# Optimization experiments

Hardware: AMD Instinct MI355X
Metric: run time of the kernel (lower is better)

## Reference

```python
import jax, jax.numpy as jnp
import numpy as np

B, C_IN, C_OUT, L = 16, 512, 512, 2048
HEADS, K, U, KS, PAD = 4, 16, 1, 3, 1
VV = C_OUT // HEADS  # 128
EPS = 1e-5


def _conv1d(x, w, pad):
    # x: [B, Cin, L], w: [Cout, Cin, KS] -> [B, Cout, L]
    return jax.lax.conv_general_dilated(
        x, w, window_strides=(1,), padding=[(pad, pad)],
        dimension_numbers=('NCH', 'OIH', 'NCH'))


def _bn_eval(y, gamma, beta, mean, var):
    # inference-mode BatchNorm1d over channel axis
    scale = gamma * jax.lax.rsqrt(var + EPS)
    shift = beta - mean * scale
    return y * scale[None, :, None] + shift[None, :, None]


def setup_inputs() -> dict:
    key = jax.random.key(0)
    ks = jax.random.split(key, 8)
    std_q = 1.0 / np.sqrt(C_IN * KS)
    x = jax.random.normal(ks[0], (B, C_IN, L), dtype=jnp.float32)
    Wq = jax.random.normal(ks[1], (K * HEADS, C_IN, KS), dtype=jnp.float32) * std_q
    Wk = jax.random.normal(ks[2], (K * U, C_IN, KS), dtype=jnp.float32) * std_q
    Wv = jax.random.normal(ks[3], (VV * U, C_IN, KS), dtype=jnp.float32) * std_q
    embedding = jax.random.normal(ks[4], (K, U), dtype=jnp.float32)
    return {
        'x': x, 'Wq': Wq,
        'q_gamma': jnp.ones((K * HEADS,), jnp.float32),
        'q_beta': jnp.zeros((K * HEADS,), jnp.float32),
        'q_mean': jnp.zeros((K * HEADS,), jnp.float32),
        'q_var': jnp.ones((K * HEADS,), jnp.float32),
        'Wk': Wk, 'Wv': Wv,
        'v_gamma': jnp.ones((VV * U,), jnp.float32),
        'v_beta': jnp.zeros((VV * U,), jnp.float32),
        'v_mean': jnp.zeros((VV * U,), jnp.float32),
        'v_var': jnp.ones((VV * U,), jnp.float32),
        'embedding': embedding,
    }


def reference(x, Wq, q_gamma, q_beta, q_mean, q_var, Wk, Wv,
              v_gamma, v_beta, v_mean, v_var, embedding):
    batch, _, n = x.shape
    # projections
    q = _bn_eval(_conv1d(x, Wq, PAD), q_gamma, q_beta, q_mean, q_var)
    q = q.reshape(batch, HEADS, K, n)                      # bhkn
    keys = _conv1d(x, Wk, PAD).reshape(batch, K, U, n)     # bkun
    sm = jax.nn.softmax(keys, axis=-1)                     # softmax over positions
    v = _bn_eval(_conv1d(x, Wv, PAD), v_gamma, v_beta, v_mean, v_var)
    v = v.reshape(batch, VV, U, n)                         # bvun
    # content lambda
    lambda_c = jnp.einsum('bkun,bvun->bkv', sm, v)
    y_c = jnp.einsum('bhkn,bkv->bhvn', q, lambda_c)
    # position lambda
    lambda_p = jnp.einsum('ku,bvun->bkvn', embedding, v)
    y_p = jnp.einsum('bhkn,bkvn->bhvn', q, lambda_p)
    out = y_c + y_p
    return out.reshape(batch, HEADS * VV, n)
```

## Files before the change

### kernel.cpp

```cpp
#include <hip/hip_runtime.h>
#include <hip/hip_bf16.h>

#define BB 16
#define CIN 512
#define LLN 2048
#define EPSV 1e-5f
#define WIMG_U16 6144

typedef __attribute__((ext_vector_type(8))) short bf16x8s;
typedef __attribute__((ext_vector_type(4))) float f32x4;

__device__ __forceinline__ unsigned short f2bf(float f) {
    union { float f; unsigned int i; } c; c.f = f;
    unsigned int x = c.i;
    unsigned int lsb = (x >> 16) & 1;
    x += 0x7fff + lsb;
    return (unsigned short)(x >> 16);
}
__device__ __forceinline__ float bf2f(unsigned short u) {
    union { unsigned int i; float f; } c; c.i = ((unsigned int)u) << 16; return c.f;
}
__device__ __forceinline__ float bflo(unsigned int w) {
    union { unsigned int i; float f; } c; c.i = w << 16; return c.f;
}
__device__ __forceinline__ float bfhi(unsigned int w) {
    union { unsigned int i; float f; } c; c.i = w & 0xffff0000u; return c.f;
}
__device__ __forceinline__ unsigned int cvtpk2(float a, float b) {
    union { __hip_bfloat162 h; unsigned int u; } c;
    c.h = __float22bfloat162_rn(float2{a, b});
    return c.u;
}

__device__ __forceinline__ void g2l16(const void* g, void* l) {
    typedef const __attribute__((address_space(1))) unsigned int GU;
    typedef __attribute__((address_space(3))) unsigned int LU;
    __builtin_amdgcn_global_load_lds((GU*)g, (LU*)l, 16, 0, 0);
}

__global__ __launch_bounds__(256) void prep_w(
    const float* __restrict__ Wq, const float* __restrict__ Wk,
    const float* __restrict__ Wv, unsigned short* __restrict__ Wpk)
{
    const int tid = threadIdx.x;
    const int wblk = blockIdx.y * 8 + blockIdx.x;
    const int img = wblk >> 1, half = wblk & 1;
    const int cot = img >> 4, chunk = img & 15;
    const int ci0 = chunk * 32;
    for (int i = half * 3072 + tid; i < half * 3072 + 3072; i += 256) {
        int t = i >> 11, r = i & 2047;
        int cf = r >> 9, lane = (r >> 3) & 63, e = i & 7;
        int lm = lane & 15, kq = lane >> 4;
        int cop = cot * 64 + cf * 16 + lm;
        int cig = ci0 + kq * 8 + e;
        float val = 0.f;
        if (cop < 64)        val = Wq[((size_t)cop * 512 + cig) * 3 + t];
        else if (cop < 80)   val = Wk[((size_t)(cop - 64) * 512 + cig) * 3 + t];
        else if (cop < 208)  val = Wv[((size_t)(cop - 80) * 512 + cig) * 3 + t];
        Wpk[(size_t)img * WIMG_U16 + i] = f2bf(val);
    }
}

__global__ __launch_bounds__(512, 4) void conv_mfma(
    const float* __restrict__ x, const unsigned short* __restrict__ Wpk,
    const float* __restrict__ qg, const float* __restrict__ qb,
    const float* __restrict__ qm, const float* __restrict__ qv,
    const float* __restrict__ vg, const float* __restrict__ vb,
    const float* __restrict__ vm, const float* __restrict__ vvar,
    unsigned short* __restrict__ qb16, float* __restrict__ kbuf,
    unsigned short* __restrict__ vb16)
{
    __shared__ __align__(16) unsigned short xT[258 * 32];
    __shared__ __align__(16) unsigned short wA[2][WIMG_U16];
    __shared__ __align__(16) float xs32[32 * 256];
    __shared__ float sscale[64], sshift[64];

    const int tid = threadIdx.x;
    const int wave = tid >> 6, lane = tid & 63;
    const int kq = lane >> 4, lm = lane & 15;
    const int n0 = blockIdx.x * 256;
    const int cot = blockIdx.y;
    const int b = blockIdx.z;

    const float* xb = x + (size_t)b * CIN * LLN;
    const unsigned short* wbase = Wpk + (size_t)cot * 16 * WIMG_U16;

    float hl0 = 0.f, hl1 = 0.f;

#define STAGE_X32(chunk)                                                        \
    {                                                                           \
        const float* src = xb + (size_t)(chunk) * 32 * LLN + n0;                \
        _Pragma("unroll")                                                       \
        for (int j = 0; j < 4; j++) {                                           \
            int i = tid + j * 512;                                              \
            g2l16(src + (size_t)(i >> 6) * LLN + (i & 63) * 4,                  \
                  (char*)xs32 + (size_t)i * 16);                                \
        }                                                                       \
    }
#define STAGE_W(buf, chunk)                                                     \
    {                                                                           \
        const unsigned short* wsrc = wbase + (size_t)(chunk) * WIMG_U16;        \
        for (int i = tid; i < 768; i += 512)                                    \
            g2l16(wsrc + (size_t)i * 8, &wA[buf][i * 8]);                       \
    }
#define HALO_ISSUE(chunk)                                                       \
    if (tid < 32) {                                                             \
        int side = tid & 1, p = tid >> 1;                                       \
        int nh = side ? (n0 + 256) : (n0 - 1);                                  \
        hl0 = 0.f; hl1 = 0.f;                                                   \
        if (nh >= 0 && nh < LLN) {                                              \
            hl0 = xb[((size_t)(chunk) * 32 + 2 * p) * LLN + nh];                \
            hl1 = xb[((size_t)(chunk) * 32 + 2 * p + 1) * LLN + nh];            \
        }                                                                       \
    }
#define TRANSPOSE()                                                             \
    {                                                                           \
        int nl = tid >> 1, h = tid & 1, rp = nl + 1;                            \
        int sig = (rp >> 1) & 3;                                                \
        unsigned short* row = &xT[rp * 32];                                     \
        _Pragma("unroll")                                                       \
        for (int g2 = 0; g2 < 2; g2++) {                                        \
            int gg = h * 2 + g2;                                                \
            float f0 = xs32[(gg * 8 + 0) * 256 + nl];                           \
            float f1 = xs32[(gg * 8 + 1) * 256 + nl];                           \
            float f2 = xs32[(gg * 8 + 2) * 256 + nl];                           \
            float f3 = xs32[(gg * 8 + 3) * 256 + nl];                           \
            float f4 = xs32[(gg * 8 + 4) * 256 + nl];                           \
            float f5 = xs32[(gg * 8 + 5) * 256 + nl];                           \
            float f6 = xs32[(gg * 8 + 6) * 256 + nl];                           \
            float f7 = xs32[(gg * 8 + 7) * 256 + nl];                           \
            uint4 w = make_uint4(cvtpk2(f0, f1), cvtpk2(f2, f3),                \
                                 cvtpk2(f4, f5), cvtpk2(f6, f7));               \
            *(uint4*)&row[(gg ^ sig) * 8] = w;                                  \
        }                                                                       \
        if (tid < 32) {                                                         \
            int side = tid & 1, p = tid >> 1;                                   \
            int hr = side ? 257 : 0;             \
            *(unsigned int*)&xT[hr * 32 + p * 2] = cvtpk2(hl0, hl1);            \
        }                                                                       \
    }

    STAGE_X32(0) STAGE_W(0, 0) HALO_ISSUE(0)

    if (tid < 64) {
        int cop = cot * 64 + tid;
        float sc = 1.f, sh = 0.f;
        if (cop < 64) {
            float g = qg[cop], be = qb[cop], m = qm[cop], va = qv[cop];
            sc = g * rsqrtf(va + EPSV); sh = be - m * sc;
        } else if (cop >= 80 && cop < 208) {
            int cc = cop - 80;
            float g = vg[cc], be = vb[cc], m = vm[cc], va = vvar[cc];
            sc = g * rsqrtf(va + EPSV); sh = be - m * sc;
        }
        sscale[tid] = sc; sshift[tid] = sh;
    }

    f32x4 acc[4][2];
#pragma unroll
    for (int i = 0; i < 4; i++)
#pragma unroll
        for (int j = 0; j < 2; j++) acc[i][j] = (f32x4){0.f, 0.f, 0.f, 0.f};

    asm volatile("s_waitcnt vmcnt(0)" ::: "memory");
    __syncthreads();
    TRANSPOSE()
    __syncthreads();

    for (int chunk = 0; chunk < 16; chunk++) {
        const int cur = chunk & 1;
        if (chunk < 15) { STAGE_X32(chunk + 1) STAGE_W(cur ^ 1, chunk + 1) HALO_ISSUE(chunk + 1) }

#pragma unroll
        for (int t = 0; t < 3; t++) {
            bf16x8s aF[4];
#pragma unroll
            for (int cf = 0; cf < 4; cf++)
                aF[cf] = *(const bf16x8s*)&wA[cur][((t * 4 + cf) * 64 + lane) * 8];
#pragma unroll
            for (int fn = 0; fn < 2; fn++) {
                int lr = wave * 32 + fn * 16 + lm + t;
                int grp = kq ^ ((lr >> 1) & 3);
                bf16x8s bF = *(const bf16x8s*)&xT[lr * 32 + grp * 8];
#pragma unroll
                for (int cf = 0; cf < 4; cf++)
                    acc[cf][fn] = __builtin_amdgcn_mfma_f32_16x16x32_bf16(
                        aF[cf], bF, acc[cf][fn], 0, 0, 0);
            }
        }
        asm volatile("s_waitcnt vmcnt(0)" ::: "memory");
        __syncthreads();
        if (chunk < 15) { TRANSPOSE() __syncthreads(); }
    }
#undef STAGE_X32
#undef STAGE_W
#undef HALO_ISSUE
#undef TRANSPOSE

#pragma unroll
    for (int cf = 0; cf < 4; cf++) {
#pragma unroll
        for (int fn = 0; fn < 2; fn++) {
#pragma unroll
            for (int r = 0; r < 4; r++) {
                int col = cf * 16 + kq * 4 + r;
                int cop = cot * 64 + col;
                if (cop >= 208) continue;
                float val = acc[cf][fn][r] * sscale[col] + sshift[col];
                int nout = n0 + wave * 32 + fn * 16 + lm;
                if (cop < 64)
                    qb16[((size_t)b * 64 + cop) * LLN + nout] = f2bf(val);
                else if (cop < 80)
                    kbuf[((size_t)b * 16 + (cop - 64)) * LLN + nout] = __expf(val - 16.f);
                else
                    vb16[((size_t)b * 128 + (cop - 80)) * LLN + nout] = f2bf(val);
            }
        }
    }
}

__global__ __launch_bounds__(256) void lambdac_kernel(
    const float* __restrict__ kexp, const unsigned short* __restrict__ vb16,
    float* __restrict__ lc2, float* __restrict__ s2)
{
    const int wave = threadIdx.x >> 6;
    const int lane = threadIdx.x & 63;
    const int idx = blockIdx.x;
    const int half = idx & 1;
    const int vgp = (idx >> 1) & 31;
    const int b = idx >> 6;
    const float* ps = kexp + ((size_t)b * 16 + wave * 4) * LLN + half * 1024;
    const unsigned short* pv = vb16 + ((size_t)b * 128 + vgp * 4) * LLN + half * 1024;

    float sum[4] = {0.f, 0.f, 0.f, 0.f};
    float acc[4][4];
#pragma unroll
    for (int k = 0; k < 4; k++)
#pragma unroll
        for (int v = 0; v < 4; v++) acc[k][v] = 0.f;
#pragma unroll
    for (int j = 0; j < 2; j++) {
        int n = (j * 64 + lane) * 8;
        float e[4][8];
#pragma unroll
        for (int k = 0; k < 4; k++) {
            float4 a = *(const float4*)&ps[(size_t)k * LLN + n];
            float4 c = *(const float4*)&ps[(size_t)k * LLN + n + 4];
            e[k][0] = a.x; e[k][1] = a.y; e[k][2] = a.z; e[k][3] = a.w;
            e[k][4] = c.x; e[k][5] = c.y; e[k][6] = c.z; e[k][7] = c.w;
            sum[k] += a.x + a.y + a.z + a.w + c.x + c.y + c.z + c.w;
        }
#pragma unroll
        for (int v = 0; v < 4; v++) {
            uint4 w = *(const uint4*)&pv[(size_t)v * LLN + n];
            float vv[8] = {bflo(w.x), bfhi(w.x), bflo(w.y), bfhi(w.y),
                           bflo(w.z), bfhi(w.z), bflo(w.w), bfhi(w.w)};
#pragma unroll
            for (int k = 0; k < 4; k++) {
                float t = 0.f;
#pragma unroll
                for (int q = 0; q < 8; q++) t += e[k][q] * vv[q];
                acc[k][v] += t;
            }
        }
    }
#pragma unroll
    for (int k = 0; k < 4; k++) {
#pragma unroll
        for (int off = 32; off > 0; off >>= 1)
            sum[k] += __shfl_xor(sum[k], off, 64);
#pragma unroll
        for (int v = 0; v < 4; v++)
#pragma unroll
            for (int off = 32; off > 0; off >>= 1)
                acc[k][v] += __shfl_xor(acc[k][v], off, 64);
    }
    if (lane == 0) {
#pragma unroll
        for (int k = 0; k < 4; k++) {
#pragma unroll
            for (int v = 0; v < 4; v++)
                lc2[(((size_t)half * 16 + b) * 16 + wave * 4 + k) * 128 + vgp * 4 + v]
                    = acc[k][v];
            if (vgp == 0)
                s2[((size_t)half * 16 + b) * 16 + wave * 4 + k] = sum[k];
        }
    }
}

__global__ __launch_bounds__(256) void final_kernel(
    const unsigned short* __restrict__ qb16, const unsigned short* __restrict__ vb16,
    const float* __restrict__ lc2, const float* __restrict__ s2,
    const float* __restrict__ emb, float* __restrict__ out)
{
    __shared__ float lcsT[64][16];
    __shared__ float es[16], invd[16];
    const int tid = threadIdx.x;
    const int h = tid >> 6, nl = tid & 63;
    const int n0 = blockIdx.x * 64;
    const int vh = blockIdx.y * 64;
    const int b = blockIdx.z;

    if (tid < 16) {
        es[tid] = emb[tid];
        invd[tid] = 1.f / (s2[(size_t)b * 16 + tid] + s2[256 + (size_t)b * 16 + tid]);
    }
    __syncthreads();
    for (int i = tid; i < 1024; i += 256) {
        int k = i & 15, vl = i >> 4;
        float l0 = lc2[((size_t)b * 16 + k) * 128 + vh + vl];
        float l1 = lc2[(size_t)32768 + ((size_t)b * 16 + k) * 128 + vh + vl];
        lcsT[vl][k] = (l0 + l1) * invd[k];
    }
    __syncthreads();

    const int n = n0 + nl;
    const unsigned short* pq = qb16 + ((size_t)b * 64 + h * 16) * LLN + n;
    float4 q4[4];
#pragma unroll
    for (int kk = 0; kk < 4; kk++) {
        q4[kk].x = bf2f(pq[(size_t)(kk * 4 + 0) * LLN]);
        q4[kk].y = bf2f(pq[(size_t)(kk * 4 + 1) * LLN]);
        q4[kk].z = bf2f(pq[(size_t)(kk * 4 + 2) * LLN]);
        q4[kk].w = bf2f(pq[(size_t)(kk * 4 + 3) * LLN]);
    }
    float s = 0.f;
#pragma unroll
    for (int kk = 0; kk < 4; kk++)
        s += q4[kk].x * es[kk * 4] + q4[kk].y * es[kk * 4 + 1]
           + q4[kk].z * es[kk * 4 + 2] + q4[kk].w * es[kk * 4 + 3];

    const unsigned short* pv = vb16 + ((size_t)b * 128 + vh) * LLN + n;
    float* po = out + ((size_t)b * 512 + h * 128 + vh) * LLN + n;
#pragma unroll 4
    for (int v = 0; v < 64; v++) {
        const float* lrow = &lcsT[v][0];
        float4 c0 = *(const float4*)&lrow[0];
        float4 c1 = *(const float4*)&lrow[4];
        float4 c2 = *(const float4*)&lrow[8];
        float4 c3 = *(const float4*)&lrow[12];
        float lam = q4[0].x * c0.x + q4[0].y * c0.y + q4[0].z * c0.z + q4[0].w * c0.w
                  + q4[1].x * c1.x + q4[1].y * c1.y + q4[1].z * c1.z + q4[1].w * c1.w
                  + q4[2].x * c2.x + q4[2].y * c2.y + q4[2].z * c2.z + q4[2].w * c2.w
                  + q4[3].x * c3.x + q4[3].y * c3.y + q4[3].z * c3.z + q4[3].w * c3.w;
        float vvv = bf2f(pv[(size_t)v * LLN]);
        po[(size_t)v * LLN] = lam + s * vvv;
    }
}

extern "C" void kernel_launch(void* const* d_in, const int* in_sizes, int n_in,
                              void* d_out, int out_size, void* d_ws, size_t ws_size,
                              hipStream_t stream)
{
    const float* x   = (const float*)d_in[0];
    const float* Wq  = (const float*)d_in[1];
    const float* qg  = (const float*)d_in[2];
    const float* qb  = (const float*)d_in[3];
    const float* qm  = (const float*)d_in[4];
    const float* qv  = (const float*)d_in[5];
    const float* Wk  = (const float*)d_in[6];
    const float* Wv  = (const float*)d_in[7];
    const float* vg  = (const float*)d_in[8];
    const float* vb  = (const float*)d_in[9];
    const float* vm  = (const float*)d_in[10];
    const float* vva = (const float*)d_in[11];
    const float* emb = (const float*)d_in[12];
    float* out = (float*)d_out;

    float* kbuf = (float*)d_ws;
    float* lc2  = kbuf + (size_t)BB * 16 * LLN;
    float* s2   = lc2 + (size_t)2 * BB * 16 * 128;
    unsigned short* qb16 = (unsigned short*)(s2 + 512);
    unsigned short* vb16 = qb16 + (size_t)BB * 64 * LLN;
    unsigned short* Wpk  = vb16 + (size_t)BB * 128 * LLN;

    hipLaunchKernelGGL(prep_w, dim3(8, 16), dim3(256), 0, stream, Wq, Wk, Wv, Wpk);

    hipLaunchKernelGGL(conv_mfma, dim3(8, 4, 16), dim3(512), 0, stream,
                       x, Wpk, qg, qb, qm, qv, vg, vb, vm, vva,
                       qb16, kbuf, vb16);

    hipLaunchKernelGGL(lambdac_kernel, dim3(1024), dim3(256), 0, stream,
                       kbuf, vb16, lc2, s2);

    hipLaunchKernelGGL(final_kernel, dim3(32, 2, BB), dim3(256), 0, stream,
                       qb16, vb16, lc2, s2, emb, out);
}
```

Baseline: 190.2 us.

## Merge lambda-content and final kernels via grid-wide atomic barrier

Fuses the lambda_c reduction kernel and the output kernel into one persistent launch of 1024 blocks. A global atomic counter, reset by the conv kernel, serves as a grid barrier between the two phases. This removes one kernel launch and the gap between launches. In exchange it relies on all 1024 blocks being co-resident, and it uses a bounded spin guard that could let a block proceed before every block has arrived, giving wrong results.

```diff
diff --git a/kernel.cpp b/kernel.cpp
--- a/kernel.cpp
+++ b/kernel.cpp
@@ -68,7 +68,7 @@
     const float* __restrict__ vg, const float* __restrict__ vb,
     const float* __restrict__ vm, const float* __restrict__ vvar,
     unsigned short* __restrict__ qb16, float* __restrict__ kbuf,
-    unsigned short* __restrict__ vb16)
+    unsigned short* __restrict__ vb16, unsigned int* __restrict__ sync_ctr)
 {
     __shared__ __align__(16) unsigned short xT[258 * 32];
     __shared__ __align__(16) unsigned short wA[2][WIMG_U16];
@@ -81,6 +81,9 @@
     const int n0 = blockIdx.x * 256;
     const int cot = blockIdx.y;
     const int b = blockIdx.z;
+
+    if (blockIdx.x == 0 && blockIdx.y == 0 && blockIdx.z == 0 && tid == 0)
+        *sync_ctr = 0;
 
     const float* xb = x + (size_t)b * CIN * LLN;
     const unsigned short* wbase = Wpk + (size_t)cot * 16 * WIMG_U16;
@@ -219,132 +222,146 @@
     }
 }
 
-__global__ __launch_bounds__(256) void lambdac_kernel(
+__global__ __launch_bounds__(256, 4) void lc_final(
     const float* __restrict__ kexp, const unsigned short* __restrict__ vb16,
-    float* __restrict__ lc2, float* __restrict__ s2)
-{
-    const int wave = threadIdx.x >> 6;
-    const int lane = threadIdx.x & 63;
-    const int idx = blockIdx.x;
-    const int half = idx & 1;
-    const int vgp = (idx >> 1) & 31;
-    const int b = idx >> 6;
-    const float* ps = kexp + ((size_t)b * 16 + wave * 4) * LLN + half * 1024;
-    const unsigned short* pv = vb16 + ((size_t)b * 128 + vgp * 4) * LLN + half * 1024;
-
-    float sum[4] = {0.f, 0.f, 0.f, 0.f};
-    float acc[4][4];
-#pragma unroll
-    for (int k = 0; k < 4; k++)
-#pragma unroll
-        for (int v = 0; v < 4; v++) acc[k][v] = 0.f;
-#pragma unroll
-    for (int j = 0; j < 2; j++) {
-        int n = (j * 64 + lane) * 8;
-        float e[4][8];
-#pragma unroll
-        for (int k = 0; k < 4; k++) {
-            float4 a = *(const float4*)&ps[(size_t)k * LLN + n];
-            float4 c = *(const float4*)&ps[(size_t)k * LLN + n + 4];
-            e[k][0] = a.x; e[k][1] = a.y; e[k][2] = a.z; e[k][3] = a.w;
-            e[k][4] = c.x; e[k][5] = c.y; e[k][6] = c.z; e[k][7] = c.w;
-            sum[k] += a.x + a.y + a.z + a.w + c.x + c.y + c.z + c.w;
-        }
-#pragma unroll
-        for (int v = 0; v < 4; v++) {
-            uint4 w = *(const uint4*)&pv[(size_t)v * LLN + n];
-            float vv[8] = {bflo(w.x), bfhi(w.x), bflo(w.y), bfhi(w.y),
-                           bflo(w.z), bfhi(w.z), bflo(w.w), bfhi(w.w)};
-#pragma unroll
-            for (int k = 0; k < 4; k++) {
-                float t = 0.f;
-#pragma unroll
-                for (int q = 0; q < 8; q++) t += e[k][q] * vv[q];
-                acc[k][v] += t;
-            }
-        }
-    }
-#pragma unroll
-    for (int k = 0; k < 4; k++) {
-#pragma unroll
-        for (int off = 32; off > 0; off >>= 1)
-            sum[k] += __shfl_xor(sum[k], off, 64);
-#pragma unroll
-        for (int v = 0; v < 4; v++)
-#pragma unroll
-            for (int off = 32; off > 0; off >>= 1)
-                acc[k][v] += __shfl_xor(acc[k][v], off, 64);
-    }
-    if (lane == 0) {
-#pragma unroll
-        for (int k = 0; k < 4; k++) {
-#pragma unroll
-            for (int v = 0; v < 4; v++)
-                lc2[(((size_t)half * 16 + b) * 16 + wave * 4 + k) * 128 + vgp * 4 + v]
-                    = acc[k][v];
-            if (vgp == 0)
-                s2[((size_t)half * 16 + b) * 16 + wave * 4 + k] = sum[k];
-        }
-    }
-}
-
-__global__ __launch_bounds__(256) void final_kernel(
-    const unsigned short* __restrict__ qb16, const unsigned short* __restrict__ vb16,
-    const float* __restrict__ lc2, const float* __restrict__ s2,
-    const float* __restrict__ emb, float* __restrict__ out)
+    const unsigned short* __restrict__ qb16, const float* __restrict__ emb,
+    float* __restrict__ lc2, float* __restrict__ s2,
+    unsigned int* __restrict__ sync_ctr, float* __restrict__ out)
 {
     __shared__ float lcsT[64][16];
     __shared__ float es[16], invd[16];
     const int tid = threadIdx.x;
-    const int h = tid >> 6, nl = tid & 63;
-    const int n0 = blockIdx.x * 64;
-    const int vh = blockIdx.y * 64;
-    const int b = blockIdx.z;
-
-    if (tid < 16) {
-        es[tid] = emb[tid];
-        invd[tid] = 1.f / (s2[(size_t)b * 16 + tid] + s2[256 + (size_t)b * 16 + tid]);
-    }
+    const int idx = blockIdx.x;
+
+    {
+        const int wave = tid >> 6;
+        const int lane = tid & 63;
+        const int half = idx & 1;
+        const int vgp = (idx >> 1) & 31;
+        const int b = idx >> 6;
+        const float* ps = kexp + ((size_t)b * 16 + wave * 4) * LLN + half * 1024;
+        const unsigned short* pv = vb16 + ((size_t)b * 128 + vgp * 4) * LLN + half * 1024;
+
+        float sum[4] = {0.f, 0.f, 0.f, 0.f};
+        float acc[4][4];
+#pragma unroll
+        for (int k = 0; k < 4; k++)
+#pragma unroll
+            for (int v = 0; v < 4; v++) acc[k][v] = 0.f;
+#pragma unroll
+        for (int j = 0; j < 2; j++) {
+            int n = (j * 64 + lane) * 8;
+            float e[4][8];
+#pragma unroll
+            for (int k = 0; k < 4; k++) {
+                float4 a = *(const float4*)&ps[(size_t)k * LLN + n];
+                float4 c = *(const float4*)&ps[(size_t)k * LLN + n + 4];
+                e[k][0] = a.x; e[k][1] = a.y; e[k][2] = a.z; e[k][3] = a.w;
+                e[k][4] = c.x; e[k][5] = c.y; e[k][6] = c.z; e[k][7] = c.w;
+                sum[k] += a.x + a.y + a.z + a.w + c.x + c.y + c.z + c.w;
+            }
+#pragma unroll
+            for (int v = 0; v < 4; v++) {
+                uint4 w = *(const uint4*)&pv[(size_t)v * LLN + n];
+                float vv[8] = {bflo(w.x), bfhi(w.x), bflo(w.y), bfhi(w.y),
+                               bflo(w.z), bfhi(w.z), bflo(w.w), bfhi(w.w)};
+#pragma unroll
+                for (int k = 0; k < 4; k++) {
+                    float t = 0.f;
+#pragma unroll
+                    for (int q = 0; q < 8; q++) t += e[k][q] * vv[q];
+                    acc[k][v] += t;
+                }
+            }
+        }
+#pragma unroll
+        for (int k = 0; k < 4; k++) {
+#pragma unroll
+            for (int off = 32; off > 0; off >>= 1)
+                sum[k] += __shfl_xor(sum[k], off, 64);
+#pragma unroll
+            for (int v = 0; v < 4; v++)
+#pragma unroll
+                for (int off = 32; off > 0; off >>= 1)
+                    acc[k][v] += __shfl_xor(acc[k][v], off, 64);
+        }
+        if (lane == 0) {
+#pragma unroll
+            for (int k = 0; k < 4; k++) {
+#pragma unroll
+                for (int v = 0; v < 4; v++)
+                    lc2[(((size_t)half * 16 + b) * 16 + wave * 4 + k) * 128 + vgp * 4 + v]
+                        = acc[k][v];
+                if (vgp == 0)
+                    s2[((size_t)half * 16 + b) * 16 + wave * 4 + k] = sum[k];
+            }
+        }
+    }
+
     __syncthreads();
-    for (int i = tid; i < 1024; i += 256) {
-        int k = i & 15, vl = i >> 4;
-        float l0 = lc2[((size_t)b * 16 + k) * 128 + vh + vl];
-        float l1 = lc2[(size_t)32768 + ((size_t)b * 16 + k) * 128 + vh + vl];
-        lcsT[vl][k] = (l0 + l1) * invd[k];
+    if (tid == 0) {
+        __threadfence();
+        atomicAdd(sync_ctr, 1u);
+        unsigned int guard = 0;
+        while (atomicAdd(sync_ctr, 0u) < 1024u && guard < (1u << 22)) {
+            ++guard;
+            __builtin_amdgcn_s_sleep(2);
+        }
+        __threadfence();
     }
     __syncthreads();
 
-    const int n = n0 + nl;
-    const unsigned short* pq = qb16 + ((size_t)b * 64 + h * 16) * LLN + n;
-    float4 q4[4];
-#pragma unroll
-    for (int kk = 0; kk < 4; kk++) {
-        q4[kk].x = bf2f(pq[(size_t)(kk * 4 + 0) * LLN]);
-        q4[kk].y = bf2f(pq[(size_t)(kk * 4 + 1) * LLN]);
-        q4[kk].z = bf2f(pq[(size_t)(kk * 4 + 2) * LLN]);
-        q4[kk].w = bf2f(pq[(size_t)(kk * 4 + 3) * LLN]);
-    }
-    float s = 0.f;
-#pragma unroll
-    for (int kk = 0; kk < 4; kk++)
-        s += q4[kk].x * es[kk * 4] + q4[kk].y * es[kk * 4 + 1]
-           + q4[kk].z * es[kk * 4 + 2] + q4[kk].w * es[kk * 4 + 3];
-
-    const unsigned short* pv = vb16 + ((size_t)b * 128 + vh) * LLN + n;
-    float* po = out + ((size_t)b * 512 + h * 128 + vh) * LLN + n;
+    {
+        const int h = tid >> 6, nl = tid & 63;
+        const int n0 = (idx & 31) * 64;
+        const int vh = ((idx >> 5) & 1) * 64;
+        const int b = idx >> 6;
+
+        if (tid < 16) {
+            es[tid] = emb[tid];
+            invd[tid] = 1.f / (s2[(size_t)b * 16 + tid] + s2[256 + (size_t)b * 16 + tid]);
+        }
+        __syncthreads();
+        for (int i = tid; i < 1024; i += 256) {
+            int k = i & 15, vl = i >> 4;
+            float l0 = lc2[((size_t)b * 16 + k) * 128 + vh + vl];
+            float l1 = lc2[(size_t)32768 + ((size_t)b * 16 + k) * 128 + vh + vl];
+            lcsT[vl][k] = (l0 + l1) * invd[k];
+        }
+        __syncthreads();
+
+        const int n = n0 + nl;
+        const unsigned short* pq = qb16 + ((size_t)b * 64 + h * 16) * LLN + n;
+        float4 q4[4];
+#pragma unroll
+        for (int kk = 0; kk < 4; kk++) {
+            q4[kk].x = bf2f(pq[(size_t)(kk * 4 + 0) * LLN]);
+            q4[kk].y = bf2f(pq[(size_t)(kk * 4 + 1) * LLN]);
+            q4[kk].z = bf2f(pq[(size_t)(kk * 4 + 2) * LLN]);
+            q4[kk].w = bf2f(pq[(size_t)(kk * 4 + 3) * LLN]);
+        }
+        float s = 0.f;
+#pragma unroll
+        for (int kk = 0; kk < 4; kk++)
+            s += q4[kk].x * es[kk * 4] + q4[kk].y * es[kk * 4 + 1]
+               + q4[kk].z * es[kk * 4 + 2] + q4[kk].w * es[kk * 4 + 3];
+
+        const unsigned short* pv = vb16 + ((size_t)b * 128 + vh) * LLN + n;
+        float* po = out + ((size_t)b * 512 + h * 128 + vh) * LLN + n;
 #pragma unroll 4
-    for (int v = 0; v < 64; v++) {
-        const float* lrow = &lcsT[v][0];
-        float4 c0 = *(const float4*)&lrow[0];
-        float4 c1 = *(const float4*)&lrow[4];
-        float4 c2 = *(const float4*)&lrow[8];
-        float4 c3 = *(const float4*)&lrow[12];
-        float lam = q4[0].x * c0.x + q4[0].y * c0.y + q4[0].z * c0.z + q4[0].w * c0.w
-                  + q4[1].x * c1.x + q4[1].y * c1.y + q4[1].z * c1.z + q4[1].w * c1.w
-                  + q4[2].x * c2.x + q4[2].y * c2.y + q4[2].z * c2.z + q4[2].w * c2.w
-                  + q4[3].x * c3.x + q4[3].y * c3.y + q4[3].z * c3.z + q4[3].w * c3.w;
-        float vvv = bf2f(pv[(size_t)v * LLN]);
-        po[(size_t)v * LLN] = lam + s * vvv;
+        for (int v = 0; v < 64; v++) {
+            const float* lrow = &lcsT[v][0];
+            float4 c0 = *(const float4*)&lrow[0];
+            float4 c1 = *(const float4*)&lrow[4];
+            float4 c2 = *(const float4*)&lrow[8];
+            float4 c3 = *(const float4*)&lrow[12];
+            float lam = q4[0].x * c0.x + q4[0].y * c0.y + q4[0].z * c0.z + q4[0].w * c0.w
+                      + q4[1].x * c1.x + q4[1].y * c1.y + q4[1].z * c1.z + q4[1].w * c1.w
+                      + q4[2].x * c2.x + q4[2].y * c2.y + q4[2].z * c2.z + q4[2].w * c2.w
+                      + q4[3].x * c3.x + q4[3].y * c3.y + q4[3].z * c3.z + q4[3].w * c3.w;
+            float vvv = bf2f(pv[(size_t)v * LLN]);
+            po[(size_t)v * LLN] = lam + s * vvv;
+        }
     }
 }
 
@@ -370,7 +387,8 @@
     float* kbuf = (float*)d_ws;
     float* lc2  = kbuf + (size_t)BB * 16 * LLN;
     float* s2   = lc2 + (size_t)2 * BB * 16 * 128;
-    unsigned short* qb16 = (unsigned short*)(s2 + 512);
+    unsigned int* ctr = (unsigned int*)(s2 + 512);
+    unsigned short* qb16 = (unsigned short*)(ctr + 16);
     unsigned short* vb16 = qb16 + (size_t)BB * 64 * LLN;
     unsigned short* Wpk  = vb16 + (size_t)BB * 128 * LLN;
 
@@ -378,11 +396,8 @@
 
     hipLaunchKernelGGL(conv_mfma, dim3(8, 4, 16), dim3(512), 0, stream,
                        x, Wpk, qg, qb, qm, qv, vg, vb, vm, vva,
-                       qb16, kbuf, vb16);
-
-    hipLaunchKernelGGL(lambdac_kernel, dim3(1024), dim3(256), 0, stream,
-                       kbuf, vb16, lc2, s2);
-
-    hipLaunchKernelGGL(final_kernel, dim3(32, 2, BB), dim3(256), 0, stream,
-                       qb16, vb16, lc2, s2, emb, out);
-}
+                       qb16, kbuf, vb16, ctr);
+
+    hipLaunchKernelGGL(lc_final, dim3(1024), dim3(256), 0, stream,
+                       kbuf, vb16, qb16, emb, lc2, s2, ctr, out);
+}
```

New measurement: 292.5 us. 53.8% more time.
